# Performance work log

Hardware: AMD Instinct MI355X
Metric: run time of the kernel (lower is better)

## Reference

```python
import jax, jax.numpy as jnp
import numpy as np

K = -1.0          # manifold curvature (hyperbolic / Poincare ball)
EPS = 1e-15

def _artanh(x):
    return jnp.arctanh(jnp.clip(x, -1.0 + 1e-7, 1.0 - 1e-7))

def _norm(x, keepdims=True):
    return jnp.sqrt(jnp.maximum(jnp.sum(x * x, axis=-1, keepdims=keepdims), EPS * EPS))

def expmap0(u):
    # sqrt(-K) == 1 for K = -1
    un = _norm(u)
    return jnp.tanh(un) * u / un

def logmap0(x):
    xn = _norm(x)
    return _artanh(xn) * x / xn

def mobius_matvec(m, x):
    xn = _norm(x)
    mx = x @ m
    mxn = _norm(mx)
    return jnp.tanh(mxn / xn * _artanh(xn)) * mx / mxn

def mobius_scalar_mul(r, x):
    xn = _norm(x)
    return jnp.tanh(r * _artanh(xn)) * x / xn

def mobius_add(x, y):
    x2 = jnp.sum(x * x, -1, keepdims=True)
    y2 = jnp.sum(y * y, -1, keepdims=True)
    xy = jnp.sum(x * y, -1, keepdims=True)
    num = (1.0 - 2.0 * K * xy - K * y2) * x + (1.0 + K * x2) * y
    den = 1.0 - 2.0 * K * xy + K * K * x2 * y2
    return num / jnp.maximum(den, EPS)

def lambda_x(x, keepdims=True):
    x2 = jnp.sum(x * x, -1, keepdims=keepdims)
    return 2.0 / jnp.maximum(1.0 + K * x2, EPS)

def kappa_layer(X, A, W):
    # mobius matvec + adjacency-weighted gyromidpoint (lincomb=True) + sigma
    XW = mobius_matvec(W, X)                       # [N, D]
    gamma = lambda_x(XW)                           # [N, 1] conformal factor
    denom = A @ (gamma - 1.0)                      # [N, 1]
    nom = A @ (gamma * XW)                         # [N, D]
    denom = jnp.where(denom >= 0, jnp.maximum(denom, 1e-10), jnp.minimum(denom, -1e-10))
    a_mean = mobius_scalar_mul(0.5, nom / denom)   # gyromidpoint
    alpha = jnp.sum(A, axis=1, keepdims=True)      # lincomb scaling
    AXW = mobius_scalar_mul(alpha, a_mean)
    return expmap0(jax.nn.relu(logmap0(AXW)))      # sigma = exp(relu(log(x)))

def get_logits(X, W, b):
    z = mobius_add(-b[None, :, :], X[:, None, :])              # [N, C, D]
    zn = jnp.maximum(_norm(z, keepdims=False), 1e-10)          # [N, C]
    an = jnp.maximum(jnp.linalg.norm(W, axis=0), 1e-10)        # [C]
    za = jnp.einsum('ncd,dc->nc', z, W)                        # [N, C]
    dist = jnp.arcsinh(2.0 * za / ((1.0 + K * zn ** 2) * an))  # arsin_k, kappa*|kappa| = -1
    lam_b = lambda_x(b, keepdims=False)                        # [C]
    return (lam_b * an) * dist

def _forward(X, A_hat, W1, W2, W_logits, p_ks):
    X = kappa_layer(X, A_hat, W1)
    X = kappa_layer(X, A_hat, W2)
    logits = get_logits(X, W_logits, p_ks)
    return A_hat @ logits                          # aggregate_logits=True


def setup_inputs() -> dict:
    key = jax.random.key(0)
    ks = jax.random.split(key, 6)
    N, D, C = 8192, 32, 16
    # node features are points on the manifold: expmap0 of small tangent vectors
    X = expmap0(jax.random.normal(ks[0], (N, D), jnp.float32) * 0.1)
    # dense non-negative normalized-adjacency-like weights, row sums ~ 1.5
    A_hat = jax.random.uniform(ks[1], (N, N), dtype=jnp.float32) * (3.0 / N)
    W1 = jax.random.normal(ks[2], (D, D), jnp.float32) * 0.01
    W2 = jax.random.normal(ks[3], (D, D), jnp.float32) * 0.01
    W_logits = jax.random.normal(ks[4], (D, C), jnp.float32) * 0.01
    p_ks = expmap0(jax.random.normal(ks[5], (C, D), jnp.float32) * 0.01)
    return {"X": X, "A_hat": A_hat, "W1": W1, "W2": W2,
            "W_logits": W_logits, "p_ks": p_ks}


def reference(X, A_hat, W1, W2, W_logits, p_ks):
    return _forward(X, A_hat, W1, W2, W_logits, p_ks)
```

## Files before the change

### kernel.cpp

```cpp
#include <hip/hip_runtime.h>

#define N_NODES 8192
#define DIM 32
#define NCLS 16
#define SPLITK 16
#define KSEG (N_NODES / SPLITK)
#define NCOLC 36
#define NKT (N_NODES / 32)
#define RT_STRIDE ((size_t)NKT * 512)
#define PITCH 520

typedef __bf16 bf16x8 __attribute__((ext_vector_type(8)));
typedef float f32x4 __attribute__((ext_vector_type(4)));

__device__ inline unsigned short f2bf(float f) {
  unsigned u = __float_as_uint(f);
  u = u + 0x7FFFu + ((u >> 16) & 1u);
  return (unsigned short)(u >> 16);
}

__device__ inline float artanh_pos(float x) {
  x = fminf(x, 1.0f - 1e-7f);
  return 0.5f * logf((1.0f + x) / (1.0f - x));
}

__device__ inline size_t g_tile_idx(int c, int n) {
  return ((size_t)(n >> 5) * 3 + (c >> 4)) * 512 + (size_t)((c & 15) * 32 + (n & 31));
}
__device__ inline size_t l_tile_idx(int c, int n) {
  return (size_t)(n >> 5) * 512 + (size_t)(c * 32 + (n & 31));
}

__global__ __launch_bounds__(256) void k_mmc(const float* __restrict__ A,
                                             const unsigned short* __restrict__ GT,
                                             unsigned short* __restrict__ Abf,
                                             float* __restrict__ Cpart) {
  __shared__ __align__(16) unsigned char ldsraw[16 * PITCH * 2];
  unsigned short* lds_t = (unsigned short*)ldsraw;
  float* lds_r = (float*)ldsraw;
  const int t = threadIdx.x;
  const int st = blockIdx.x;
  const int rt = st >> 4;
  const int ks = st & 15;
  const int lane = t & 63;
  const int w = t >> 6;
  const int lr = lane & 15;
  const int lkg = lane >> 4;

  const float* src = A + (size_t)(rt * 16) * N_NODES + ks * 512;
#pragma unroll
  for (int v = 0; v < 8; v++) {
    const int row = 2 * v + (t >> 7);
    const int k = (t & 127) * 4;
    f32x4 f = __builtin_nontemporal_load((const f32x4*)(src + (size_t)row * N_NODES + k));
    uint2 o;
    o.x = f2bf(f[0]) | ((unsigned)f2bf(f[1]) << 16);
    o.y = f2bf(f[2]) | ((unsigned)f2bf(f[3]) << 16);
    *(uint2*)(lds_t + row * PITCH + k) = o;
  }
  __syncthreads();

  f32x4 acc[3];
#pragma unroll
  for (int nf = 0; nf < 3; nf++) acc[nf] = (f32x4){0.f, 0.f, 0.f, 0.f};
  const int poff = lr * 32 + lkg * 8;
#pragma unroll
  for (int i = 0; i < 4; i++) {
    const int kt2 = 4 * w + i;
    bf16x8 a = *(const bf16x8*)(lds_t + lr * PITCH + kt2 * 32 + lkg * 8);
#pragma unroll
    for (int nf = 0; nf < 3; nf++) {
      bf16x8 b = *(const bf16x8*)(GT + ((size_t)(ks * 16 + kt2) * 3 + nf) * 512 + poff);
      acc[nf] = __builtin_amdgcn_mfma_f32_16x16x32_bf16(a, b, acc[nf], 0, 0, 0);
    }
  }

  unsigned short* dst = Abf + (size_t)st * 8192;
#pragma unroll
  for (int u = 0; u < 4; u++) {
    const int p = u * 256 + t;
    const int kt = p >> 6;
    const int q = p & 63;
    const int row = q >> 2;
    const int kl = (q & 3) * 8;
    bf16x8 val = *(const bf16x8*)(lds_t + row * PITCH + kt * 32 + kl);
    *(bf16x8*)(dst + (size_t)p * 8) = val;
  }
  __syncthreads();

#pragma unroll
  for (int nf = 0; nf < 3; nf++)
#pragma unroll
    for (int j = 0; j < 4; j++)
      lds_r[(w * 16 + lkg * 4 + j) * 48 + nf * 16 + lr] = acc[nf][j];
  __syncthreads();

  for (int e = t; e < 16 * 36; e += 256) {
    const int row = e / 36;
    const int col = e % 36;
    float s = lds_r[row * 48 + col] + lds_r[768 + row * 48 + col] +
              lds_r[1536 + row * 48 + col] + lds_r[2304 + row * 48 + col];
    Cpart[((size_t)ks * N_NODES + rt * 16 + row) * NCOLC + col] = s;
  }
}

__device__ inline void pre_math(const float* __restrict__ Wl, const float x[DIM],
                                unsigned short* __restrict__ GT, int n) {
  float xn2 = 0.f;
#pragma unroll
  for (int i = 0; i < DIM; i++) xn2 += x[i] * x[i];
  float xn = sqrtf(fmaxf(xn2, 1e-30f));
  float mx[DIM];
#pragma unroll
  for (int j = 0; j < DIM; j++) mx[j] = 0.f;
  for (int i = 0; i < DIM; i++) {
    float xi = x[i];
#pragma unroll
    for (int j = 0; j < DIM; j++) mx[j] = fmaf(xi, Wl[i * DIM + j], mx[j]);
  }
  float mxn2 = 0.f;
#pragma unroll
  for (int j = 0; j < DIM; j++) mxn2 += mx[j] * mx[j];
  float mxn = sqrtf(fmaxf(mxn2, 1e-30f));
  float t = tanhf(mxn / xn * artanh_pos(xn));
  float sc = t / mxn;
  float xw[DIM];
  float x2n = 0.f;
#pragma unroll
  for (int j = 0; j < DIM; j++) { xw[j] = sc * mx[j]; x2n += xw[j] * xw[j]; }
  float gamma = 2.0f / fmaxf(1.0f - x2n, 1e-15f);
#pragma unroll
  for (int c = 0; c < DIM; c++) GT[g_tile_idx(c, n)] = f2bf(gamma * xw[c]);
  GT[g_tile_idx(32, n)] = f2bf(gamma - 1.0f);
  GT[g_tile_idx(33, n)] = f2bf(1.0f);
#pragma unroll
  for (int c = DIM + 2; c < 48; c++) GT[g_tile_idx(c, n)] = 0;
}

__global__ void k_pre1(const float* __restrict__ X, const float* __restrict__ W,
                       unsigned short* __restrict__ GT) {
  __shared__ float Wl[DIM * DIM];
  for (int i = threadIdx.x; i < DIM * DIM; i += blockDim.x) Wl[i] = W[i];
  __syncthreads();
  const int n = blockIdx.x * blockDim.x + threadIdx.x;
  float x[DIM];
#pragma unroll
  for (int i = 0; i < DIM; i += 4) {
    float4 v = *(const float4*)(X + (size_t)n * DIM + i);
    x[i] = v.x; x[i + 1] = v.y; x[i + 2] = v.z; x[i + 3] = v.w;
  }
  pre_math(Wl, x, GT, n);
}

__device__ inline void post_math(const float* __restrict__ Cpart, int n, float xo[DIM]) {
  float acc[NCOLC];
#pragma unroll
  for (int c = 0; c < NCOLC; c++) acc[c] = 0.f;
  for (int s = 0; s < SPLITK; s++) {
    const float4* p = (const float4*)(Cpart + ((size_t)s * N_NODES + n) * NCOLC);
#pragma unroll
    for (int q = 0; q < NCOLC / 4; q++) {
      float4 v = p[q];
      acc[q * 4 + 0] += v.x; acc[q * 4 + 1] += v.y;
      acc[q * 4 + 2] += v.z; acc[q * 4 + 3] += v.w;
    }
  }
  float denom = acc[32];
  float alpha = acc[33];
  denom = (denom >= 0.f) ? fmaxf(denom, 1e-10f) : fminf(denom, -1e-10f);
  float inv = 1.0f / denom;
  float v[DIM];
  float vn2 = 0.f;
#pragma unroll
  for (int c = 0; c < DIM; c++) { v[c] = acc[c] * inv; vn2 += v[c] * v[c]; }
  float vn = sqrtf(fmaxf(vn2, 1e-30f));
  float un = alpha * 0.5f * artanh_pos(vn);
  float su = un / vn;
  float r[DIM];
  float rn2 = 0.f;
#pragma unroll
  for (int c = 0; c < DIM; c++) { r[c] = fmaxf(su * v[c], 0.f); rn2 += r[c] * r[c]; }
  float rn = sqrtf(fmaxf(rn2, 1e-30f));
  float so = tanhf(rn) / rn;
#pragma unroll
  for (int c = 0; c < DIM; c++) xo[c] = so * r[c];
}

__global__ void k_postpre(const float* __restrict__ Cpart, const float* __restrict__ W,
                          unsigned short* __restrict__ GT) {
  __shared__ float Wl[DIM * DIM];
  for (int i = threadIdx.x; i < DIM * DIM; i += blockDim.x) Wl[i] = W[i];
  __syncthreads();
  const int n = blockIdx.x * blockDim.x + threadIdx.x;
  float x[DIM];
  post_math(Cpart, n, x);
  pre_math(Wl, x, GT, n);
}

__global__ void k_postlogits(const float* __restrict__ Cpart, const float* __restrict__ Wl_g,
                             const float* __restrict__ B_g, unsigned short* __restrict__ LT) {
  __shared__ float Wc[DIM * NCLS];
  __shared__ float Bc[NCLS * DIM];
  __shared__ float an_s[NCLS], lam_s[NCLS], b2_s[NCLS];
  for (int i = threadIdx.x; i < DIM * NCLS; i += blockDim.x) { Wc[i] = Wl_g[i]; Bc[i] = B_g[i]; }
  __syncthreads();
  if (threadIdx.x < NCLS) {
    int c = threadIdx.x;
    float b2 = 0.f, w2 = 0.f;
    for (int d = 0; d < DIM; d++) {
      b2 += Bc[c * DIM + d] * Bc[c * DIM + d];
      w2 += Wc[d * NCLS + c] * Wc[d * NCLS + c];
    }
    b2_s[c] = b2;
    an_s[c] = fmaxf(sqrtf(w2), 1e-10f);
    lam_s[c] = 2.0f / fmaxf(1.0f - b2, 1e-15f);
  }
  __syncthreads();
  const int n = blockIdx.x * blockDim.x + threadIdx.x;
  float x[DIM];
  post_math(Cpart, n, x);
  float y2 = 0.f;
#pragma unroll
  for (int i = 0; i < DIM; i++) y2 += x[i] * x[i];
  for (int c = 0; c < NCLS; c++) {
    float b2 = b2_s[c];
    float bx = 0.f;
    for (int d = 0; d < DIM; d++) bx += Bc[c * DIM + d] * x[d];
    float xy = -bx;
    float f1 = 1.0f + 2.0f * xy + y2;
    float f2 = 1.0f - b2;
    float den = fmaxf(1.0f + 2.0f * xy + b2 * y2, 1e-15f);
    float invden = 1.0f / den;
    float zn2 = 0.f, za = 0.f;
    for (int d = 0; d < DIM; d++) {
      float z = (f1 * (-Bc[c * DIM + d]) + f2 * x[d]) * invden;
      zn2 += z * z;
      za += z * Wc[d * NCLS + c];
    }
    float zn = fmaxf(sqrtf(fmaxf(zn2, 1e-30f)), 1e-10f);
    float dist = asinhf(2.0f * za / ((1.0f - zn * zn) * an_s[c]));
    LT[l_tile_idx(c, n)] = f2bf(lam_s[c] * an_s[c] * dist);
  }
}

template <int NF>
__global__ __launch_bounds__(256) void k_mm(const unsigned short* __restrict__ A,
                                            const unsigned short* __restrict__ BT,
                                            float* __restrict__ Cpart) {
  const int lane = threadIdx.x & 63;
  const int wid = threadIdx.x >> 6;
  const int r0 = blockIdx.x * 128 + wid * 32;
  const int kt0 = blockIdx.y * (KSEG / 32);
  const int lr = lane & 15;
  const int lkg = lane >> 4;
  const int poff = lr * 32 + lkg * 8;
  const int BS = (NF == 3) ? 3 : 1;
  f32x4 acc[2][NF];
#pragma unroll
  for (int m = 0; m < 2; m++)
#pragma unroll
    for (int nf = 0; nf < NF; nf++) acc[m][nf] = (f32x4){0.f, 0.f, 0.f, 0.f};
  const unsigned short* pa0 = A + ((size_t)(r0 >> 4) * NKT + kt0) * 512 + poff;
  const unsigned short* pa1 = pa0 + RT_STRIDE;
  const unsigned short* pbB = BT + (size_t)kt0 * BS * 512 + poff;
#pragma unroll 4
  for (int kt = 0; kt < KSEG / 32; kt++) {
    bf16x8 a0 = *(const bf16x8*)(pa0 + (size_t)kt * 512);
    bf16x8 a1 = *(const bf16x8*)(pa1 + (size_t)kt * 512);
#pragma unroll
    for (int nf = 0; nf < NF; nf++) {
      bf16x8 b = *(const bf16x8*)(pbB + (size_t)(kt * BS + nf) * 512);
      acc[0][nf] = __builtin_amdgcn_mfma_f32_16x16x32_bf16(a0, b, acc[0][nf], 0, 0, 0);
      acc[1][nf] = __builtin_amdgcn_mfma_f32_16x16x32_bf16(a1, b, acc[1][nf], 0, 0, 0);
    }
  }
  const int NCOL = (NF == 3) ? NCOLC : NF * 16;
  float* Cb = Cpart + (size_t)blockIdx.y * N_NODES * NCOL;
#pragma unroll
  for (int m = 0; m < 2; m++)
#pragma unroll
    for (int nf = 0; nf < NF; nf++) {
      if (NF == 3 && nf == 2 && lr >= 4) continue;
#pragma unroll
      for (int j = 0; j < 4; j++) {
        int row = r0 + m * 16 + lkg * 4 + j;
        int col = nf * 16 + lr;
        Cb[(size_t)row * NCOL + col] = acc[m][nf][j];
      }
    }
}

template <int TOTAL>
__global__ void k_red(const float* __restrict__ part, float* __restrict__ outb) {
  int i = blockIdx.x * blockDim.x + threadIdx.x;
  if (i < TOTAL) {
    float s = 0.f;
#pragma unroll
    for (int q = 0; q < SPLITK; q++) s += part[(size_t)q * TOTAL + i];
    outb[i] = s;
  }
}

extern "C" void kernel_launch(void* const* d_in, const int* in_sizes, int n_in,
                              void* d_out, int out_size, void* d_ws, size_t ws_size,
                              hipStream_t stream) {
  (void)in_sizes; (void)n_in; (void)out_size; (void)ws_size;
  const float* X  = (const float*)d_in[0];
  const float* A  = (const float*)d_in[1];
  const float* W1 = (const float*)d_in[2];
  const float* W2 = (const float*)d_in[3];
  const float* WL = (const float*)d_in[4];
  const float* PK = (const float*)d_in[5];
  float* out = (float*)d_out;

  char* ws = (char*)d_ws;
  unsigned short* Abf = (unsigned short*)ws;
  unsigned short* GT  = (unsigned short*)(ws + 134217728);
  float* Cpart        = (float*)(ws + 135004160);
  unsigned short* LT  = (unsigned short*)(ws + 153878528);

  k_pre1<<<N_NODES / 64, 64, 0, stream>>>(X, W1, GT);
  k_mmc<<<8192, 256, 0, stream>>>(A, GT, Abf, Cpart);
  k_postpre<<<N_NODES / 64, 64, 0, stream>>>(Cpart, W2, GT);

  k_mm<3><<<dim3(64, SPLITK), 256, 0, stream>>>(Abf, GT, Cpart);
  k_postlogits<<<N_NODES / 64, 64, 0, stream>>>(Cpart, WL, PK, LT);

  k_mm<1><<<dim3(64, SPLITK), 256, 0, stream>>>(Abf, LT, Cpart);
  k_red<N_NODES * NCLS><<<N_NODES * NCLS / 256, 256, 0, stream>>>(Cpart, out);
}
```

Measured before the change: 182.0 us.

## Recompute from fp32 adjacency each pass instead of caching a bf16 copy

Removes the bf16 copy of A written in the first pass and the separate bf16 matmul kernel. Each of the three adjacency products now re-streams the fp32 A through one templated kernel that converts to bf16 in LDS. Each wave writes its own partial result, so the in-block LDS reduction is dropped and the split count rises to 64. This cuts the 128MB bf16 write but reads fp32 A three times and makes the partial buffers four times larger for the post and reduce kernels to read.

```diff
diff --git a/kernel.cpp b/kernel.cpp
--- a/kernel.cpp
+++ b/kernel.cpp
@@ -3,11 +3,8 @@
 #define N_NODES 8192
 #define DIM 32
 #define NCLS 16
-#define SPLITK 16
-#define KSEG (N_NODES / SPLITK)
+#define SPLITC 64
 #define NCOLC 36
-#define NKT (N_NODES / 32)
-#define RT_STRIDE ((size_t)NKT * 512)
 #define PITCH 520
 
 typedef __bf16 bf16x8 __attribute__((ext_vector_type(8)));
@@ -31,13 +28,11 @@
   return (size_t)(n >> 5) * 512 + (size_t)(c * 32 + (n & 31));
 }
 
-__global__ __launch_bounds__(256) void k_mmc(const float* __restrict__ A,
-                                             const unsigned short* __restrict__ GT,
-                                             unsigned short* __restrict__ Abf,
+template <int NF>
+__global__ __launch_bounds__(256) void k_mmA(const float* __restrict__ A,
+                                             const unsigned short* __restrict__ BT,
                                              float* __restrict__ Cpart) {
-  __shared__ __align__(16) unsigned char ldsraw[16 * PITCH * 2];
-  unsigned short* lds_t = (unsigned short*)ldsraw;
-  float* lds_r = (float*)ldsraw;
+  __shared__ __align__(16) unsigned short lds_t[16 * PITCH];
   const int t = threadIdx.x;
   const int st = blockIdx.x;
   const int rt = st >> 4;
@@ -48,59 +43,50 @@
   const int lkg = lane >> 4;
 
   const float* src = A + (size_t)(rt * 16) * N_NODES + ks * 512;
+  f32x4 r[8];
 #pragma unroll
   for (int v = 0; v < 8; v++) {
     const int row = 2 * v + (t >> 7);
     const int k = (t & 127) * 4;
-    f32x4 f = __builtin_nontemporal_load((const f32x4*)(src + (size_t)row * N_NODES + k));
+    r[v] = __builtin_nontemporal_load((const f32x4*)(src + (size_t)row * N_NODES + k));
+  }
+#pragma unroll
+  for (int v = 0; v < 8; v++) {
+    const int row = 2 * v + (t >> 7);
+    const int k = (t & 127) * 4;
     uint2 o;
-    o.x = f2bf(f[0]) | ((unsigned)f2bf(f[1]) << 16);
-    o.y = f2bf(f[2]) | ((unsigned)f2bf(f[3]) << 16);
+    o.x = f2bf(r[v][0]) | ((unsigned)f2bf(r[v][1]) << 16);
+    o.y = f2bf(r[v][2]) | ((unsigned)f2bf(r[v][3]) << 16);
     *(uint2*)(lds_t + row * PITCH + k) = o;
   }
   __syncthreads();
 
-  f32x4 acc[3];
-#pragma unroll
-  for (int nf = 0; nf < 3; nf++) acc[nf] = (f32x4){0.f, 0.f, 0.f, 0.f};
+  f32x4 acc[NF];
+#pragma unroll
+  for (int nf = 0; nf < NF; nf++) acc[nf] = (f32x4){0.f, 0.f, 0.f, 0.f};
   const int poff = lr * 32 + lkg * 8;
 #pragma unroll
   for (int i = 0; i < 4; i++) {
     const int kt2 = 4 * w + i;
     bf16x8 a = *(const bf16x8*)(lds_t + lr * PITCH + kt2 * 32 + lkg * 8);
 #pragma unroll
-    for (int nf = 0; nf < 3; nf++) {
-      bf16x8 b = *(const bf16x8*)(GT + ((size_t)(ks * 16 + kt2) * 3 + nf) * 512 + poff);
+    for (int nf = 0; nf < NF; nf++) {
+      bf16x8 b = *(const bf16x8*)(BT + ((size_t)(ks * 16 + kt2) * NF + nf) * 512 + poff);
       acc[nf] = __builtin_amdgcn_mfma_f32_16x16x32_bf16(a, b, acc[nf], 0, 0, 0);
     }
   }
 
-  unsigned short* dst = Abf + (size_t)st * 8192;
-#pragma unroll
-  for (int u = 0; u < 4; u++) {
-    const int p = u * 256 + t;
-    const int kt = p >> 6;
-    const int q = p & 63;
-    const int row = q >> 2;
-    const int kl = (q & 3) * 8;
-    bf16x8 val = *(const bf16x8*)(lds_t + row * PITCH + kt * 32 + kl);
-    *(bf16x8*)(dst + (size_t)p * 8) = val;
-  }
-  __syncthreads();
-
-#pragma unroll
-  for (int nf = 0; nf < 3; nf++)
-#pragma unroll
-    for (int j = 0; j < 4; j++)
-      lds_r[(w * 16 + lkg * 4 + j) * 48 + nf * 16 + lr] = acc[nf][j];
-  __syncthreads();
-
-  for (int e = t; e < 16 * 36; e += 256) {
-    const int row = e / 36;
-    const int col = e % 36;
-    float s = lds_r[row * 48 + col] + lds_r[768 + row * 48 + col] +
-              lds_r[1536 + row * 48 + col] + lds_r[2304 + row * 48 + col];
-    Cpart[((size_t)ks * N_NODES + rt * 16 + row) * NCOLC + col] = s;
+  const int NCOL = (NF == 3) ? NCOLC : 16;
+  float* Cb = Cpart + (size_t)(ks * 4 + w) * N_NODES * NCOL;
+#pragma unroll
+  for (int nf = 0; nf < NF; nf++) {
+    if (NF == 3 && nf == 2 && lr >= 4) continue;
+#pragma unroll
+    for (int j = 0; j < 4; j++) {
+      const int row = rt * 16 + lkg * 4 + j;
+      const int col = nf * 16 + lr;
+      Cb[(size_t)row * NCOL + col] = acc[nf][j];
+    }
   }
 }
 
@@ -156,7 +142,7 @@
   float acc[NCOLC];
 #pragma unroll
   for (int c = 0; c < NCOLC; c++) acc[c] = 0.f;
-  for (int s = 0; s < SPLITK; s++) {
+  for (int s = 0; s < SPLITC; s++) {
     const float4* p = (const float4*)(Cpart + ((size_t)s * N_NODES + n) * NCOLC);
 #pragma unroll
     for (int q = 0; q < NCOLC / 4; q++) {
@@ -243,60 +229,13 @@
   }
 }
 
-template <int NF>
-__global__ __launch_bounds__(256) void k_mm(const unsigned short* __restrict__ A,
-                                            const unsigned short* __restrict__ BT,
-                                            float* __restrict__ Cpart) {
-  const int lane = threadIdx.x & 63;
-  const int wid = threadIdx.x >> 6;
-  const int r0 = blockIdx.x * 128 + wid * 32;
-  const int kt0 = blockIdx.y * (KSEG / 32);
-  const int lr = lane & 15;
-  const int lkg = lane >> 4;
-  const int poff = lr * 32 + lkg * 8;
-  const int BS = (NF == 3) ? 3 : 1;
-  f32x4 acc[2][NF];
-#pragma unroll
-  for (int m = 0; m < 2; m++)
-#pragma unroll
-    for (int nf = 0; nf < NF; nf++) acc[m][nf] = (f32x4){0.f, 0.f, 0.f, 0.f};
-  const unsigned short* pa0 = A + ((size_t)(r0 >> 4) * NKT + kt0) * 512 + poff;
-  const unsigned short* pa1 = pa0 + RT_STRIDE;
-  const unsigned short* pbB = BT + (size_t)kt0 * BS * 512 + poff;
-#pragma unroll 4
-  for (int kt = 0; kt < KSEG / 32; kt++) {
-    bf16x8 a0 = *(const bf16x8*)(pa0 + (size_t)kt * 512);
-    bf16x8 a1 = *(const bf16x8*)(pa1 + (size_t)kt * 512);
-#pragma unroll
-    for (int nf = 0; nf < NF; nf++) {
-      bf16x8 b = *(const bf16x8*)(pbB + (size_t)(kt * BS + nf) * 512);
-      acc[0][nf] = __builtin_amdgcn_mfma_f32_16x16x32_bf16(a0, b, acc[0][nf], 0, 0, 0);
-      acc[1][nf] = __builtin_amdgcn_mfma_f32_16x16x32_bf16(a1, b, acc[1][nf], 0, 0, 0);
-    }
-  }
-  const int NCOL = (NF == 3) ? NCOLC : NF * 16;
-  float* Cb = Cpart + (size_t)blockIdx.y * N_NODES * NCOL;
-#pragma unroll
-  for (int m = 0; m < 2; m++)
-#pragma unroll
-    for (int nf = 0; nf < NF; nf++) {
-      if (NF == 3 && nf == 2 && lr >= 4) continue;
-#pragma unroll
-      for (int j = 0; j < 4; j++) {
-        int row = r0 + m * 16 + lkg * 4 + j;
-        int col = nf * 16 + lr;
-        Cb[(size_t)row * NCOL + col] = acc[m][nf][j];
-      }
-    }
-}
-
 template <int TOTAL>
 __global__ void k_red(const float* __restrict__ part, float* __restrict__ outb) {
   int i = blockIdx.x * blockDim.x + threadIdx.x;
   if (i < TOTAL) {
     float s = 0.f;
 #pragma unroll
-    for (int q = 0; q < SPLITK; q++) s += part[(size_t)q * TOTAL + i];
+    for (int q = 0; q < SPLITC; q++) s += part[(size_t)q * TOTAL + i];
     outb[i] = s;
   }
 }
@@ -314,18 +253,17 @@
   float* out = (float*)d_out;
 
   char* ws = (char*)d_ws;
-  unsigned short* Abf = (unsigned short*)ws;
-  unsigned short* GT  = (unsigned short*)(ws + 134217728);
-  float* Cpart        = (float*)(ws + 135004160);
-  unsigned short* LT  = (unsigned short*)(ws + 153878528);
+  unsigned short* GT = (unsigned short*)ws;
+  unsigned short* LT = (unsigned short*)(ws + 786432);
+  float* Cpart       = (float*)(ws + 1048576);
 
   k_pre1<<<N_NODES / 64, 64, 0, stream>>>(X, W1, GT);
-  k_mmc<<<8192, 256, 0, stream>>>(A, GT, Abf, Cpart);
+  k_mmA<3><<<8192, 256, 0, stream>>>(A, GT, Cpart);
   k_postpre<<<N_NODES / 64, 64, 0, stream>>>(Cpart, W2, GT);
 
-  k_mm<3><<<dim3(64, SPLITK), 256, 0, stream>>>(Abf, GT, Cpart);
+  k_mmA<3><<<8192, 256, 0, stream>>>(A, GT, Cpart);
   k_postlogits<<<N_NODES / 64, 64, 0, stream>>>(Cpart, WL, PK, LT);
 
-  k_mm<1><<<dim3(64, SPLITK), 256, 0, stream>>>(Abf, LT, Cpart);
-  k_red<N_NODES * NCLS><<<N_NODES * NCLS / 256, 256, 0, stream>>>(Cpart, out);
-}
+  k_mmA<1><<<8192, 256, 0, stream>>>(A, LT, Cpart);
+  k_red<N_NODES * NCLS><<<(N_NODES * NCLS + 255) / 256, 256, 0, stream>>>(Cpart, out);
+}
```

Result: slower. 288.2 us (+58.4%).

## Process two K-segments per block in k_mmc with software-pipelined loads

Applied to the files above, without the earlier changes.

Each k_mmc block now handles two adjacent 512-wide K segments of the same 16-row tile. It issues the global loads for the second segment before running the MFMAs and bf16 write-out of the first, using two LDS buffers. This halves the grid and the number of split-K partials (8 instead of 16), so k_postpre reduces fewer partial rows. The cost is more registers and LDS per block, which may lower occupancy on what is mostly a bandwidth-bound fp32 stream of A.

```diff
diff --git a/kernel.cpp b/kernel.cpp
--- a/kernel.cpp
+++ b/kernel.cpp
@@ -3,12 +3,11 @@
 #define N_NODES 8192
 #define DIM 32
 #define NCLS 16
-#define SPLITK 16
-#define KSEG (N_NODES / SPLITK)
 #define NCOLC 36
 #define NKT (N_NODES / 32)
 #define RT_STRIDE ((size_t)NKT * 512)
 #define PITCH 520
+#define KSEG 512
 
 typedef __bf16 bf16x8 __attribute__((ext_vector_type(8)));
 typedef float f32x4 __attribute__((ext_vector_type(4)));
@@ -35,56 +34,97 @@
                                              const unsigned short* __restrict__ GT,
                                              unsigned short* __restrict__ Abf,
                                              float* __restrict__ Cpart) {
-  __shared__ __align__(16) unsigned char ldsraw[16 * PITCH * 2];
-  unsigned short* lds_t = (unsigned short*)ldsraw;
-  float* lds_r = (float*)ldsraw;
+  __shared__ __align__(16) unsigned short buf0[16 * PITCH];
+  __shared__ __align__(16) unsigned short buf1[16 * PITCH];
+  float* lds_r = (float*)buf0;
   const int t = threadIdx.x;
-  const int st = blockIdx.x;
-  const int rt = st >> 4;
-  const int ks = st & 15;
+  const int rt = blockIdx.x >> 3;
+  const int q = blockIdx.x & 7;
+  const int ks0 = 2 * q, ks1 = 2 * q + 1;
   const int lane = t & 63;
   const int w = t >> 6;
   const int lr = lane & 15;
   const int lkg = lane >> 4;
-
-  const float* src = A + (size_t)(rt * 16) * N_NODES + ks * 512;
+  const int vrow = t >> 7;
+  const int vk = (t & 127) * 4;
+  const int poff = lr * 32 + lkg * 8;
+
+  const float* srcbase = A + (size_t)(rt * 16) * N_NODES;
+
+  f32x4 r0[8];
+#pragma unroll
+  for (int v = 0; v < 8; v++)
+    r0[v] = __builtin_nontemporal_load(
+        (const f32x4*)(srcbase + (size_t)(2 * v + vrow) * N_NODES + ks0 * KSEG + vk));
 #pragma unroll
   for (int v = 0; v < 8; v++) {
-    const int row = 2 * v + (t >> 7);
-    const int k = (t & 127) * 4;
-    f32x4 f = __builtin_nontemporal_load((const f32x4*)(src + (size_t)row * N_NODES + k));
     uint2 o;
-    o.x = f2bf(f[0]) | ((unsigned)f2bf(f[1]) << 16);
-    o.y = f2bf(f[2]) | ((unsigned)f2bf(f[3]) << 16);
-    *(uint2*)(lds_t + row * PITCH + k) = o;
-  }
-  __syncthreads();
+    o.x = f2bf(r0[v][0]) | ((unsigned)f2bf(r0[v][1]) << 16);
+    o.y = f2bf(r0[v][2]) | ((unsigned)f2bf(r0[v][3]) << 16);
+    *(uint2*)(buf0 + (2 * v + vrow) * PITCH + vk) = o;
+  }
+  __syncthreads();
+
+  f32x4 r1[8];
+#pragma unroll
+  for (int v = 0; v < 8; v++)
+    r1[v] = __builtin_nontemporal_load(
+        (const f32x4*)(srcbase + (size_t)(2 * v + vrow) * N_NODES + ks1 * KSEG + vk));
 
   f32x4 acc[3];
 #pragma unroll
   for (int nf = 0; nf < 3; nf++) acc[nf] = (f32x4){0.f, 0.f, 0.f, 0.f};
-  const int poff = lr * 32 + lkg * 8;
 #pragma unroll
   for (int i = 0; i < 4; i++) {
     const int kt2 = 4 * w + i;
-    bf16x8 a = *(const bf16x8*)(lds_t + lr * PITCH + kt2 * 32 + lkg * 8);
+    bf16x8 a = *(const bf16x8*)(buf0 + lr * PITCH + kt2 * 32 + lkg * 8);
 #pragma unroll
     for (int nf = 0; nf < 3; nf++) {
-      bf16x8 b = *(const bf16x8*)(GT + ((size_t)(ks * 16 + kt2) * 3 + nf) * 512 + poff);
+      bf16x8 b = *(const bf16x8*)(GT + ((size_t)(ks0 * 16 + kt2) * 3 + nf) * 512 + poff);
       acc[nf] = __builtin_amdgcn_mfma_f32_16x16x32_bf16(a, b, acc[nf], 0, 0, 0);
     }
   }
-
-  unsigned short* dst = Abf + (size_t)st * 8192;
-#pragma unroll
-  for (int u = 0; u < 4; u++) {
-    const int p = u * 256 + t;
-    const int kt = p >> 6;
-    const int q = p & 63;
-    const int row = q >> 2;
-    const int kl = (q & 3) * 8;
-    bf16x8 val = *(const bf16x8*)(lds_t + row * PITCH + kt * 32 + kl);
-    *(bf16x8*)(dst + (size_t)p * 8) = val;
+  {
+    unsigned short* dst = Abf + (size_t)(rt * 16 + ks0) * 8192;
+#pragma unroll
+    for (int u = 0; u < 4; u++) {
+      const int p = u * 256 + t;
+      const int kt = p >> 6;
+      const int qq = p & 63;
+      bf16x8 val = *(const bf16x8*)(buf0 + (qq >> 2) * PITCH + kt * 32 + (qq & 3) * 8);
+      *(bf16x8*)(dst + (size_t)p * 8) = val;
+    }
+  }
+
+#pragma unroll
+  for (int v = 0; v < 8; v++) {
+    uint2 o;
+    o.x = f2bf(r1[v][0]) | ((unsigned)f2bf(r1[v][1]) << 16);
+    o.y = f2bf(r1[v][2]) | ((unsigned)f2bf(r1[v][3]) << 16);
+    *(uint2*)(buf1 + (2 * v + vrow) * PITCH + vk) = o;
+  }
+  __syncthreads();
+
+#pragma unroll
+  for (int i = 0; i < 4; i++) {
+    const int kt2 = 4 * w + i;
+    bf16x8 a = *(const bf16x8*)(buf1 + lr * PITCH + kt2 * 32 + lkg * 8);
+#pragma unroll
+    for (int nf = 0; nf < 3; nf++) {
+      bf16x8 b = *(const bf16x8*)(GT + ((size_t)(ks1 * 16 + kt2) * 3 + nf) * 512 + poff);
+      acc[nf] = __builtin_amdgcn_mfma_f32_16x16x32_bf16(a, b, acc[nf], 0, 0, 0);
+    }
+  }
+  {
+    unsigned short* dst = Abf + (size_t)(rt * 16 + ks1) * 8192;
+#pragma unroll
+    for (int u = 0; u < 4; u++) {
+      const int p = u * 256 + t;
+      const int kt = p >> 6;
+      const int qq = p & 63;
+      bf16x8 val = *(const bf16x8*)(buf1 + (qq >> 2) * PITCH + kt * 32 + (qq & 3) * 8);
+      *(bf16x8*)(dst + (size_t)p * 8) = val;
+    }
   }
   __syncthreads();
 
@@ -94,13 +134,12 @@
     for (int j = 0; j < 4; j++)
       lds_r[(w * 16 + lkg * 4 + j) * 48 + nf * 16 + lr] = acc[nf][j];
   __syncthreads();
-
   for (int e = t; e < 16 * 36; e += 256) {
     const int row = e / 36;
     const int col = e % 36;
     float s = lds_r[row * 48 + col] + lds_r[768 + row * 48 + col] +
               lds_r[1536 + row * 48 + col] + lds_r[2304 + row * 48 + col];
-    Cpart[((size_t)ks * N_NODES + rt * 16 + row) * NCOLC + col] = s;
+    Cpart[((size_t)q * N_NODES + rt * 16 + row) * NCOLC + col] = s;
   }
 }
 
@@ -152,17 +191,18 @@
   pre_math(Wl, x, GT, n);
 }
 
+template <int SPLITS>
 __device__ inline void post_math(const float* __restrict__ Cpart, int n, float xo[DIM]) {
   float acc[NCOLC];
 #pragma unroll
   for (int c = 0; c < NCOLC; c++) acc[c] = 0.f;
-  for (int s = 0; s < SPLITK; s++) {
+  for (int s = 0; s < SPLITS; s++) {
     const float4* p = (const float4*)(Cpart + ((size_t)s * N_NODES + n) * NCOLC);
 #pragma unroll
-    for (int q = 0; q < NCOLC / 4; q++) {
-      float4 v = p[q];
-      acc[q * 4 + 0] += v.x; acc[q * 4 + 1] += v.y;
-      acc[q * 4 + 2] += v.z; acc[q * 4 + 3] += v.w;
+    for (int qq = 0; qq < NCOLC / 4; qq++) {
+      float4 v = p[qq];
+      acc[qq * 4 + 0] += v.x; acc[qq * 4 + 1] += v.y;
+      acc[qq * 4 + 2] += v.z; acc[qq * 4 + 3] += v.w;
     }
   }
   float denom = acc[32];
@@ -193,7 +233,7 @@
   __syncthreads();
   const int n = blockIdx.x * blockDim.x + threadIdx.x;
   float x[DIM];
-  post_math(Cpart, n, x);
+  post_math<8>(Cpart, n, x);
   pre_math(Wl, x, GT, n);
 }
 
@@ -218,7 +258,7 @@
   __syncthreads();
   const int n = blockIdx.x * blockDim.x + threadIdx.x;
   float x[DIM];
-  post_math(Cpart, n, x);
+  post_math<16>(Cpart, n, x);
   float y2 = 0.f;
 #pragma unroll
   for (int i = 0; i < DIM; i++) y2 += x[i] * x[i];
@@ -250,7 +290,7 @@
   const int lane = threadIdx.x & 63;
   const int wid = threadIdx.x >> 6;
   const int r0 = blockIdx.x * 128 + wid * 32;
-  const int kt0 = blockIdx.y * (KSEG / 32);
+  const int kt0 = blockIdx.y * (512 / 32);
   const int lr = lane & 15;
   const int lkg = lane >> 4;
   const int poff = lr * 32 + lkg * 8;
@@ -264,7 +304,7 @@
   const unsigned short* pa1 = pa0 + RT_STRIDE;
   const unsigned short* pbB = BT + (size_t)kt0 * BS * 512 + poff;
 #pragma unroll 4
-  for (int kt = 0; kt < KSEG / 32; kt++) {
+  for (int kt = 0; kt < 16; kt++) {
     bf16x8 a0 = *(const bf16x8*)(pa0 + (size_t)kt * 512);
     bf16x8 a1 = *(const bf16x8*)(pa1 + (size_t)kt * 512);
 #pragma unroll
@@ -290,13 +330,13 @@
     }
 }
 
-template <int TOTAL>
+template <int TOTAL, int SPLITS>
 __global__ void k_red(const float* __restrict__ part, float* __restrict__ outb) {
   int i = blockIdx.x * blockDim.x + threadIdx.x;
   if (i < TOTAL) {
     float s = 0.f;
 #pragma unroll
-    for (int q = 0; q < SPLITK; q++) s += part[(size_t)q * TOTAL + i];
+    for (int qq = 0; qq < SPLITS; qq++) s += part[(size_t)qq * TOTAL + i];
     outb[i] = s;
   }
 }
@@ -320,12 +360,12 @@
   unsigned short* LT  = (unsigned short*)(ws + 153878528);
 
   k_pre1<<<N_NODES / 64, 64, 0, stream>>>(X, W1, GT);
-  k_mmc<<<8192, 256, 0, stream>>>(A, GT, Abf, Cpart);
+  k_mmc<<<4096, 256, 0, stream>>>(A, GT, Abf, Cpart);
   k_postpre<<<N_NODES / 64, 64, 0, stream>>>(Cpart, W2, GT);
 
-  k_mm<3><<<dim3(64, SPLITK), 256, 0, stream>>>(Abf, GT, Cpart);
+  k_mm<3><<<dim3(64, 16), 256, 0, stream>>>(Abf, GT, Cpart);
   k_postlogits<<<N_NODES / 64, 64, 0, stream>>>(Cpart, WL, PK, LT);
 
-  k_mm<1><<<dim3(64, SPLITK), 256, 0, stream>>>(Abf, LT, Cpart);
-  k_red<N_NODES * NCLS><<<N_NODES * NCLS / 256, 256, 0, stream>>>(Cpart, out);
-}
+  k_mm<1><<<dim3(64, 16), 256, 0, stream>>>(Abf, LT, Cpart);
+  k_red<N_NODES * NCLS, 16><<<(N_NODES * NCLS + 255) / 256, 256, 0, stream>>>(Cpart, out);
+}
```

Measured after the change: 181.3 us. Within noise of the previous version (-0.4%).
